# Kernel optimization log

Hardware: AMD Instinct MI355X
Metric: run time of the kernel (lower is better)

The kernel has to match this reference:

```python
import jax, jax.numpy as jnp
import numpy as np

B, A, G = 8, 200000, 64
K = 4                       # max_k: top-k anchors per GT
T_LOW, T_HIGH = 0.3, 0.7    # matcher thresholds
NUM_SAMPLES, POS_FRAC = 256, 0.5  # batch_size_per_image, positive_fraction
MAX_POS = int(NUM_SAMPLES * POS_FRAC)  # 128


def cxcywh_to_xyxy(b):
    cx, cy, w, h = b[..., 0], b[..., 1], b[..., 2], b[..., 3]
    return jnp.stack([cx - 0.5 * w, cy - 0.5 * h, cx + 0.5 * w, cy + 0.5 * h], axis=-1)


def box_iou(b1, b2):
    # b1: [G,4], b2: [A,4] in xyxy -> iou [G,A]
    area1 = (b1[:, 2] - b1[:, 0]) * (b1[:, 3] - b1[:, 1])
    area2 = (b2[:, 2] - b2[:, 0]) * (b2[:, 3] - b2[:, 1])
    lt = jnp.maximum(b1[:, None, :2], b2[None, :, :2])
    rb = jnp.minimum(b1[:, None, 2:], b2[None, :, 2:])
    wh = jnp.clip(rb - lt, 0.0)
    inter = wh[..., 0] * wh[..., 1]
    union = area1[:, None] + area2[None, :] - inter
    return inter / union


def _per_image(anchors, gt, key):
    iou = box_iou(cxcywh_to_xyxy(gt), cxcywh_to_xyxy(anchors))  # [G, A]
    # --- Matcher(thresholds=[t_low, t_high], labels=[0,-1,1], allow_low_quality_matches=True)
    matched_vals = iou.max(axis=0)        # best IoU per anchor
    matches = jnp.argmax(iou, axis=0)     # matched GT per anchor
    labels = jnp.where(matched_vals >= T_HIGH, 1,
             jnp.where(matched_vals >= T_LOW, -1, 0))
    hq = iou.max(axis=1)                  # highest quality per GT
    labels = jnp.where((iou == hq[:, None]).any(axis=0), 1, labels)  # low-quality matches -> positive
    # --- subsample_labels: randomly keep at most 128 positives (negatives don't affect outputs)
    is_pos = labels == 1
    r = jax.random.uniform(key, (anchors.shape[0],))
    rank = jnp.argsort(jnp.argsort(jnp.where(is_pos, r, 2.0)))  # random rank among positives
    num_pos = jnp.minimum(MAX_POS, is_pos.sum())
    sel_pos = is_pos & (rank < num_pos)
    # --- sample_topk_per_gt: per GT keep min(count, K) top-IoU anchors (fixed-shape, padded with -1)
    counts = jax.ops.segment_sum(sel_pos.astype(jnp.int32), matches, num_segments=G)
    top_vals, top_idx = jax.lax.top_k(iou, K)  # [G, K]
    valid = jnp.arange(K)[None, :] < jnp.minimum(counts, K)[:, None]
    pr = jnp.where(valid, top_idx, -1).reshape(-1)
    gt_i = jnp.where(valid, jnp.arange(G)[:, None], -1).reshape(-1)
    scores = jnp.where(valid, top_vals, 0.0).reshape(-1)
    return pr, gt_i, valid.reshape(-1), scores


def setup_inputs() -> dict:
    key = jax.random.key(0)
    k1, k2 = jax.random.split(key)
    anchors = jax.random.uniform(k1, (B, A, 4), dtype=jnp.float32)   # cxcywh
    gt_boxes = jax.random.uniform(k2, (B, G, 4), dtype=jnp.float32)  # cxcywh
    return {"anchors": anchors, "gt_boxes": gt_boxes}


def reference(anchors, gt_boxes):
    # Returns padded (pr_inds, gt_inds, valid_mask, topk_ious), each [B, G*K];
    # invalid slots hold -1 indices (padding for the variable-length torch output).
    keys = jax.random.split(jax.random.key(42), anchors.shape[0])
    return jax.vmap(_per_image)(anchors, gt_boxes, keys)
```

## Files before the change

### kernel.cpp

```cpp
#include <hip/hip_runtime.h>
#include <stdint.h>


#pragma clang fp contract(off)

#define B_IMG 8
#define A_N 200000
#define G_N 64
#define K_TOP 4
#define MAX_POS 128
#define FINE_CAP 4096
#define AS 2048
#define NS 98
#define SUB_SL 16
#define SUB_AS 1024
#define WPS 32
#define NWORD 3136

typedef unsigned long long u64;
typedef unsigned int u32;

__device__ __forceinline__ u32 rotl32(u32 v, int n) { return (v << n) | (v >> (32 - n)); }

__device__ __forceinline__ void tf_round(u32& x0, u32& x1, int r) {
  x0 += x1; x1 = rotl32(x1, r); x1 ^= x0;
}

__device__ __forceinline__ void threefry2x32(u32 k0, u32 k1, u32& x0, u32& x1) {
  u32 ks2 = 0x1BD11BDAu ^ k0 ^ k1;
  x0 += k0; x1 += k1;
  tf_round(x0,x1,13); tf_round(x0,x1,15); tf_round(x0,x1,26); tf_round(x0,x1,6);
  x0 += k1; x1 += ks2 + 1u;
  tf_round(x0,x1,17); tf_round(x0,x1,29); tf_round(x0,x1,16); tf_round(x0,x1,24);
  x0 += ks2; x1 += k0 + 2u;
  tf_round(x0,x1,13); tf_round(x0,x1,15); tf_round(x0,x1,26); tf_round(x0,x1,6);
  x0 += k0; x1 += k1 + 3u;
  tf_round(x0,x1,17); tf_round(x0,x1,29); tf_round(x0,x1,16); tf_round(x0,x1,24);
  x0 += k1; x1 += ks2 + 4u;
  tf_round(x0,x1,13); tf_round(x0,x1,15); tf_round(x0,x1,26); tf_round(x0,x1,6);
  x0 += ks2; x1 += k0 + 5u;
}

__device__ __forceinline__ void image_key(int b, u32& kb0, u32& kb1) {
  u32 x0 = 0u, x1 = (u32)b;
  threefry2x32(0u, 42u, x0, x1);
  kb0 = x0; kb1 = x1;
}

__device__ __forceinline__ u32 rbits_for(u32 k0, u32 k1, u32 a) {
  u32 x0 = 0u, x1 = a;
  threefry2x32(k0, k1, x0, x1);
  return x0 ^ x1;
}

__device__ __forceinline__ void conv_box(float4 bx, float& x0, float& y0,
                                         float& x1, float& y1, float& area) {
  #pragma clang fp contract(off)
  x0 = bx.x - 0.5f * bx.z;
  y0 = bx.y - 0.5f * bx.w;
  x1 = bx.x + 0.5f * bx.z;
  y1 = bx.y + 0.5f * bx.w;
  area = (x1 - x0) * (y1 - y0);
}

__device__ __forceinline__ float iou_pair(float ax0, float ay0, float ax1, float ay1, float aarea,
                                          float gx0, float gy0, float gx1, float gy1, float garea) {
  #pragma clang fp contract(off)
  float ltx = fmaxf(gx0, ax0), lty = fmaxf(gy0, ay0);
  float rbx = fminf(gx1, ax1), rby = fminf(gy1, ay1);
  float w = fmaxf(rbx - ltx, 0.0f), h = fmaxf(rby - lty, 0.0f);
  float inter = w * h;
  float uni = (garea + aarea) - inter;
  return inter / uni;
}

__device__ __forceinline__ void iou_parts(float ax0, float ay0, float ax1, float ay1, float aarea,
                                          float gx0, float gy0, float gx1, float gy1, float garea,
                                          float& inter, float& uni) {
  #pragma clang fp contract(off)
  float ltx = fmaxf(gx0, ax0), lty = fmaxf(gy0, ay0);
  float rbx = fminf(gx1, ax1), rby = fminf(gy1, ay1);
  float w = fmaxf(rbx - ltx, 0.0f), h = fmaxf(rby - lty, 0.0f);
  inter = w * h;
  uni = (garea + aarea) - inter;
}

__device__ __forceinline__ void top4_insert(u64 (&top)[4], u64 key) {
  if (key > top[3]) {
    if (key > top[0])      { top[3]=top[2]; top[2]=top[1]; top[1]=top[0]; top[0]=key; }
    else if (key > top[1]) { top[3]=top[2]; top[2]=top[1]; top[1]=key; }
    else if (key > top[2]) { top[3]=top[2]; top[2]=key; }
    else                   { top[3]=key; }
  }
}

__device__ __forceinline__ void wave_merge_top4(u64 (&top)[4]) {
  for (int off = 32; off >= 1; off >>= 1) {
    u64 o[4];
    #pragma unroll
    for (int k = 0; k < 4; k++) o[k] = __shfl_down(top[k], (unsigned)off);
    u64 m[4]; int i = 0, j = 0;
    #pragma unroll
    for (int k = 0; k < 4; k++) m[k] = (top[i] >= o[j]) ? top[i++] : o[j++];
    #pragma unroll
    for (int k = 0; k < 4; k++) top[k] = m[k];
  }
}

__device__ __forceinline__ void wave_merge_top4_u32(u32 (&top)[4]) {
  for (int off = 32; off >= 1; off >>= 1) {
    u32 o[4];
    #pragma unroll
    for (int k = 0; k < 4; k++) o[k] = __shfl_down(top[k], (unsigned)off);
    u32 m[4]; int i = 0, j = 0;
    #pragma unroll
    for (int k = 0; k < 4; k++) m[k] = (top[i] >= o[j]) ? top[i++] : o[j++];
    #pragma unroll
    for (int k = 0; k < 4; k++) top[k] = m[k];
  }
}

__device__ __forceinline__ float screen_thresh(u32 tau) {
  u32 tb = (tau > 8u) ? (tau - 8u) : 0u;
  return __uint_as_float(tb);
}

__launch_bounds__(512, 4)
__global__ void k_thresh(const float4* __restrict__ anchors, const float4* __restrict__ gt,
                         u32* __restrict__ thr_part, u32* __restrict__ hist,
                         u32* __restrict__ npos, u32* __restrict__ fcnt,
                         u32* __restrict__ cnt,
                         float* __restrict__ out, int sec) {
  const int s = blockIdx.x;
  const int b = blockIdx.y;
  const int half = blockIdx.z;
  const int t = threadIdx.x;
  const int wave = t >> 6, lane = t & 63;

  __shared__ float4 sxy[SUB_AS];
  __shared__ float  sg[5][32];

  {
    int lid = ((half * B_IMG + b) * SUB_SL + s) * 512 + t;
    if (lid < B_IMG * 4096) hist[lid] = 0;
    if (lid < B_IMG * G_N * K_TOP) {
      out[0 * sec + lid] = -1.0f;
      out[1 * sec + lid] = -1.0f;
      out[2 * sec + lid] = 0.0f;
      out[3 * sec + lid] = 0.0f;
    }
  }
  if (s == 0 && half == 0) {
    if (t < 64) cnt[b * G_N + t] = 0;
    if (t == 0) { fcnt[b] = 0; npos[b] = 0; }
  }

  const int base = s * SUB_AS;
  const float4* ab = anchors + (size_t)b * A_N + base;

  for (int j = t; j < SUB_AS; j += 512) {
    float x0, y0, x1, y1, ar;
    conv_box(ab[j], x0, y0, x1, y1, ar);
    sxy[j] = make_float4(x0, y0, x1, y1);
  }
  if (t < 32) {
    float x0, y0, x1, y1, ar;
    conv_box(gt[(size_t)b * G_N + half * 32 + t], x0, y0, x1, y1, ar);
    sg[0][t] = x0; sg[1][t] = y0; sg[2][t] = x1; sg[3][t] = y1; sg[4][t] = ar;
  }
  __syncthreads();

  {
    const int gi = wave * 4;
    const float g0x0 = sg[0][gi],   g0y0 = sg[1][gi],   g0x1 = sg[2][gi],   g0y1 = sg[3][gi],   g0a = sg[4][gi];
    const float g1x0 = sg[0][gi+1], g1y0 = sg[1][gi+1], g1x1 = sg[2][gi+1], g1y1 = sg[3][gi+1], g1a = sg[4][gi+1];
    const float g2x0 = sg[0][gi+2], g2y0 = sg[1][gi+2], g2x1 = sg[2][gi+2], g2y1 = sg[3][gi+2], g2a = sg[4][gi+2];
    const float g3x0 = sg[0][gi+3], g3y0 = sg[1][gi+3], g3x1 = sg[2][gi+3], g3y1 = sg[3][gi+3], g3a = sg[4][gi+3];

    u32 q0 = 0, q1 = 0, q2 = 0, q3 = 0;
    for (int j = lane; j < SUB_AS; j += 64) {
      float4 x = sxy[j];
      float aarea = (x.z - x.x) * (x.w - x.y);
      float i0, u0, i1, u1, i2, u2, i3, u3;
      iou_parts(x.x, x.y, x.z, x.w, aarea, g0x0, g0y0, g0x1, g0y1, g0a, i0, u0);
      iou_parts(x.x, x.y, x.z, x.w, aarea, g1x0, g1y0, g1x1, g1y1, g1a, i1, u1);
      iou_parts(x.x, x.y, x.z, x.w, aarea, g2x0, g2y0, g2x1, g2y1, g2a, i2, u2);
      iou_parts(x.x, x.y, x.z, x.w, aarea, g3x0, g3y0, g3x1, g3y1, g3a, i3, u3);
      q0 = max(q0, __float_as_uint(i0 * __builtin_amdgcn_rcpf(u0)));
      q1 = max(q1, __float_as_uint(i1 * __builtin_amdgcn_rcpf(u1)));
      q2 = max(q2, __float_as_uint(i2 * __builtin_amdgcn_rcpf(u2)));
      q3 = max(q3, __float_as_uint(i3 * __builtin_amdgcn_rcpf(u3)));
    }
    u32 Q0[4] = {q0,0,0,0}, Q1[4] = {q1,0,0,0}, Q2[4] = {q2,0,0,0}, Q3[4] = {q3,0,0,0};
    wave_merge_top4_u32(Q0);
    wave_merge_top4_u32(Q1);
    wave_merge_top4_u32(Q2);
    wave_merge_top4_u32(Q3);
    if (lane == 0) {
      u32* dst = thr_part + ((size_t)b * SUB_SL + s) * G_N + half * 32 + gi;
      dst[0] = Q0[3]; dst[1] = Q1[3]; dst[2] = Q2[3]; dst[3] = Q3[3];
    }
  }
}

__launch_bounds__(512, 4)
__global__ void k_main(const float4* __restrict__ anchors, const float4* __restrict__ gt,
                       const u32* __restrict__ thr_part,
                       u64* __restrict__ partial, u64* __restrict__ posA,
                       u32* __restrict__ hist, u32* __restrict__ npos) {
  const int s = blockIdx.x;
  const int b = blockIdx.y;
  const int t = threadIdx.x;
  const int wave = t >> 6, lane = t & 63;

  __shared__ float4 sxy[AS];
  __shared__ float  sg[5][64];
  __shared__ float  sthr[64];
  u32* wm = (u32*)sxy;

  const int base = s * AS;
  const int acnt = min(AS, A_N - base);
  const float4* ab = anchors + (size_t)b * A_N + base;

  for (int j = t; j < acnt; j += 512) {
    float x0, y0, x1, y1, ar;
    conv_box(ab[j], x0, y0, x1, y1, ar);
    sxy[j] = make_float4(x0, y0, x1, y1);
  }
  if (t < 64) {
    float x0, y0, x1, y1, ar;
    conv_box(gt[(size_t)b * G_N + t], x0, y0, x1, y1, ar);
    sg[0][t] = x0; sg[1][t] = y0; sg[2][t] = x1; sg[3][t] = y1; sg[4][t] = ar;
    u32 mx = 0;
    for (int ss = 0; ss < SUB_SL; ss++)
      mx = max(mx, thr_part[((size_t)b * SUB_SL + ss) * G_N + t]);
    const u32 L7 = 0x3F333333u - 8u;
    sthr[t] = screen_thresh(min(mx > 16u ? mx - 16u : 0u, L7));
  }
  __syncthreads();

  u32 m = 0;
  for (int gg = 0; gg < 2; gg++) {
    const int gp = wave * 2 + gg;
    const int gi = gp * 4;
    const float g0x0 = sg[0][gi],   g0y0 = sg[1][gi],   g0x1 = sg[2][gi],   g0y1 = sg[3][gi],   g0a = sg[4][gi];
    const float g1x0 = sg[0][gi+1], g1y0 = sg[1][gi+1], g1x1 = sg[2][gi+1], g1y1 = sg[3][gi+1], g1a = sg[4][gi+1];
    const float g2x0 = sg[0][gi+2], g2y0 = sg[1][gi+2], g2x1 = sg[2][gi+2], g2y1 = sg[3][gi+2], g2a = sg[4][gi+2];
    const float g3x0 = sg[0][gi+3], g3y0 = sg[1][gi+3], g3x1 = sg[2][gi+3], g3y1 = sg[3][gi+3], g3a = sg[4][gi+3];
    const float t0 = sthr[gi], t1 = sthr[gi+1], t2 = sthr[gi+2], t3 = sthr[gi+3];

    u64 T0[4] = {0,0,0,0}, T1[4] = {0,0,0,0}, T2[4] = {0,0,0,0}, T3[4] = {0,0,0,0};
    u32 h0 = 0, h1 = 0, h2 = 0, h3 = 0;
    u32 bit = 1u;
    for (int j = lane; j < acnt; j += 64, bit <<= 1) {
      float4 x = sxy[j];
      float aarea = (x.z - x.x) * (x.w - x.y);
      float i0, u0, i1, u1, i2, u2, i3, u3;
      iou_parts(x.x, x.y, x.z, x.w, aarea, g0x0, g0y0, g0x1, g0y1, g0a, i0, u0);
      iou_parts(x.x, x.y, x.z, x.w, aarea, g1x0, g1y0, g1x1, g1y1, g1a, i1, u1);
      iou_parts(x.x, x.y, x.z, x.w, aarea, g2x0, g2y0, g2x1, g2y1, g2a, i2, u2);
      iou_parts(x.x, x.y, x.z, x.w, aarea, g3x0, g3y0, g3x1, g3y1, g3a, i3, u3);
      u32 ni = ~(u32)(base + j);
      bool s0 = (i0 >= t0 * u0), s1 = (i1 >= t1 * u1);
      bool s2 = (i2 >= t2 * u2), s3 = (i3 >= t3 * u3);
      if (__ballot(s0)) {
        float v = 0.0f;
        if (s0) { v = i0 / u0; if (v >= 0.7f) m |= bit; }
        u32 vb = __float_as_uint(v);
        bool ins = s0 && (vb >= h0);
        if (__ballot(ins)) {
          if (ins) top4_insert(T0, ((u64)vb << 32) | (u64)ni);
          h0 = (u32)(T0[3] >> 32);
        }
      }
      if (__ballot(s1)) {
        float v = 0.0f;
        if (s1) { v = i1 / u1; if (v >= 0.7f) m |= bit; }
        u32 vb = __float_as_uint(v);
        bool ins = s1 && (vb >= h1);
        if (__ballot(ins)) {
          if (ins) top4_insert(T1, ((u64)vb << 32) | (u64)ni);
          h1 = (u32)(T1[3] >> 32);
        }
      }
      if (__ballot(s2)) {
        float v = 0.0f;
        if (s2) { v = i2 / u2; if (v >= 0.7f) m |= bit; }
        u32 vb = __float_as_uint(v);
        bool ins = s2 && (vb >= h2);
        if (__ballot(ins)) {
          if (ins) top4_insert(T2, ((u64)vb << 32) | (u64)ni);
          h2 = (u32)(T2[3] >> 32);
        }
      }
      if (__ballot(s3)) {
        float v = 0.0f;
        if (s3) { v = i3 / u3; if (v >= 0.7f) m |= bit; }
        u32 vb = __float_as_uint(v);
        bool ins = s3 && (vb >= h3);
        if (__ballot(ins)) {
          if (ins) top4_insert(T3, ((u64)vb << 32) | (u64)ni);
          h3 = (u32)(T3[3] >> 32);
        }
      }
    }
    wave_merge_top4(T0);
    wave_merge_top4(T1);
    wave_merge_top4(T2);
    wave_merge_top4(T3);
    if (lane == 0) {
      u64* dst = partial + (((size_t)b * NS + s) * G_N + gi) * 4;
      #pragma unroll
      for (int k = 0; k < 4; k++) {
        dst[k] = T0[k]; dst[4 + k] = T1[k]; dst[8 + k] = T2[k]; dst[12 + k] = T3[k];
      }
    }
  }

  __syncthreads();
  wm[t] = m;
  __syncthreads();
  if (wave == 0) {
    u32 mc = 0;
    #pragma unroll
    for (int w = 0; w < 8; w++) mc |= wm[w * 64 + lane];
    u64* posH = posA + (size_t)b * NWORD + s * WPS;
    for (int k = 0; k < WPS; k++) {
      u64 bal = __ballot((mc >> k) & 1u);
      if (lane == 0) posH[k] = bal;
    }
    u32 k0, k1; image_key(b, k0, k1);
    u32 c = (u32)__popc(mc);
    u32 mm = mc;
    while (mm) {
      int k = __ffs((int)mm) - 1; mm &= mm - 1;
      u32 a = (u32)(base + k * 64 + lane);
      atomicAdd(&hist[b * 4096 + (rbits_for(k0, k1, a) >> 20)], 1u);
    }
    #pragma unroll
    for (int off = 32; off >= 1; off >>= 1) c += __shfl_xor(c, off);
    if (lane == 0 && c) atomicAdd(&npos[b], c);
  }
}

__launch_bounds__(64)
__global__ void k_top4_merge(const u64* __restrict__ partial, u64* __restrict__ top4,
                             u64* __restrict__ posA,
                             u32* __restrict__ hist, u32* __restrict__ npos) {
  const int b = blockIdx.y, g = blockIdx.x, lane = threadIdx.x;
  const u64* pb = partial + ((size_t)b * NS * G_N + g) * 4;
  u64 keys[7];
  int nk = 0;
  for (int i = lane; i < NS * 4; i += 64)
    keys[nk++] = pb[(size_t)(i >> 2) * (G_N * 4) + (i & 3)];
  u64 top[4] = {0ull, 0ull, 0ull, 0ull};
  for (int q = 0; q < nk; q++) top4_insert(top, keys[q]);
  wave_merge_top4(top);
  if (lane == 0) {
    u64* dst = top4 + ((size_t)b * G_N + g) * 4;
    #pragma unroll
    for (int k = 0; k < 4; k++) dst[k] = top[k];
  }
  u32 hqb = (u32)(__shfl(top[0], 0) >> 32);
  u32 kk0, kk1; image_key(b, kk0, kk1);
  for (int q = 0; q < nk; q++) {
    u64 key = keys[q];
    u32 aidx = ~(u32)key;
    if ((u32)(key >> 32) == hqb && aidx < A_N) {
      u64 bit = 1ull << (aidx & 63);
      u64 old = atomicOr(&posA[(size_t)b * NWORD + (aidx >> 6)], bit);
      if (!(old & bit)) {
        atomicAdd(&hist[b * 4096 + (rbits_for(kk0, kk1, aidx) >> 20)], 1u);
        atomicAdd(&npos[b], 1u);
      }
    }
  }
}

__launch_bounds__(256)
__global__ void k_collect(const u64* __restrict__ posA,
                          const u32* __restrict__ npos, const u32* __restrict__ hist,
                          int2* __restrict__ binsel,
                          u32* __restrict__ fine, u32* __restrict__ fcnt) {
  const int b = blockIdx.y;
  const int t = threadIdx.x;
  __shared__ u32 red[256];
  __shared__ int sbin;

  const u32* hb = hist + b * 4096;
  u32 local = 0;
  for (int j = 0; j < 16; j++) local += hb[t * 16 + j];
  red[t] = local;
  __syncthreads();
  if (t == 0) {
    if (npos[b] <= MAX_POS) {
      sbin = -1;
      binsel[b] = make_int2(-1, 0);
    } else {
      u32 cum = 0; int chunk = 0;
      for (int i = 0; i < 256; i++) {
        if (cum + red[i] >= MAX_POS) { chunk = i; break; }
        cum += red[i];
      }
      int tb = chunk * 16; u32 before = cum;
      for (int j = 0; j < 16; j++) {
        u32 h = hb[chunk * 16 + j];
        if (before + h >= MAX_POS) { tb = chunk * 16 + j; break; }
        before += h;
      }
      sbin = tb;
      binsel[b] = make_int2(tb, (int)before);
    }
  }
  __syncthreads();
  const int stb = sbin;
  if (stb < 0) return;

  u32 k0, k1; image_key(b, k0, k1);
  const int a0 = blockIdx.x * AS;
  const u64* pa = posA + (size_t)b * NWORD;
  for (int j = t; j < AS; j += 256) {
    int a = a0 + j;
    if (a >= A_N) break;
    if (!((pa[a >> 6] >> (a & 63)) & 1ull)) continue;
    u32 rb = rbits_for(k0, k1, (u32)a);
    if ((int)(rb >> 20) != stb) continue;
    u32 idx = atomicAdd(&fcnt[b], 1u);
    if (idx < FINE_CAP) fine[b * FINE_CAP + idx] = (((rb >> 9) & 0x7FFu) << 18) | (u32)a;
  }
}

__launch_bounds__(256)
__global__ void k_count(const float4* __restrict__ anchors, const float4* __restrict__ gt,
                        const u64* __restrict__ posA,
                        const int2* __restrict__ binsel, const u32* __restrict__ fine,
                        const u32* __restrict__ fcnt, u32* __restrict__ cnt,
                        const u64* __restrict__ top4,
                        float* __restrict__ out, int sec) {
  const int b = blockIdx.y;
  const int t = threadIdx.x;
  __shared__ float sg[5][64];
  __shared__ u64 sT;

  if (t < 64) {
    float x0, y0, x1, y1, ar;
    conv_box(gt[(size_t)b * G_N + t], x0, y0, x1, y1, ar);
    sg[0][t] = x0; sg[1][t] = y0; sg[2][t] = x1; sg[3][t] = y1; sg[4][t] = ar;
    int2 bs = binsel[b];
    u64 T = ~0ull;
    if (bs.x >= 0) {
      const int m = min((int)fcnt[b], FINE_CAP);
      const u32 need = (u32)(MAX_POS - bs.y);
      const u32* fb = fine + b * FINE_CAP;
      u32 lo = 0, hi = (1u << 29) - 1;
      while (lo < hi) {
        u32 mid = lo + ((hi - lo) >> 1);
        u32 c = 0;
        for (int j = t; j < m; j += 64) c += (fb[j] <= mid) ? 1u : 0u;
        #pragma unroll
        for (int off = 32; off >= 1; off >>= 1) c += __shfl_xor(c, off);
        if (c >= need) hi = mid; else lo = mid + 1;
      }
      T = ((u64)(u32)bs.x << 29) | (u64)lo;
    }
    if (t == 0) sT = T;
  }
  __syncthreads();

  u32 k0, k1; image_key(b, k0, k1);
  const u64 T = sT;
  const int a0 = blockIdx.x * AS;
  const u64* pa = posA + (size_t)b * NWORD;
  const float4* ab = anchors + (size_t)b * A_N;
  for (int j = t; j < AS; j += 256) {
    int a = a0 + j;
    if (a >= A_N) break;
    if (!((pa[a >> 6] >> (a & 63)) & 1ull)) continue;
    if (T != ~0ull) {
      u32 rb = rbits_for(k0, k1, (u32)a);
      if (((((u64)(rb >> 9)) << 18) | (u64)(u32)a) > T) continue;
    }
    float ax0, ay0, ax1, ay1, aar;
    conv_box(ab[a], ax0, ay0, ax1, ay1, aar);
    float bv = -1.0f; int g0 = 0;
    for (int g = 0; g < 64; g++) {
      float v = iou_pair(ax0, ay0, ax1, ay1, aar,
                         sg[0][g], sg[1][g], sg[2][g], sg[3][g], sg[4][g]);
      if (v > bv) { bv = v; g0 = g; }
    }
    u32 r = atomicAdd(&cnt[b * G_N + g0], 1u);
    if (r < (u32)K_TOP) {
      u64 key = top4[((size_t)b * G_N + g0) * 4 + r];
      u32 fb4 = (u32)(key >> 32);
      u32 aidx = ~(u32)key;
      int o = b * (G_N * K_TOP) + g0 * K_TOP + (int)r;
      out[0 * sec + o] = (float)aidx;
      out[1 * sec + o] = (float)g0;
      out[2 * sec + o] = 1.0f;
      out[3 * sec + o] = __uint_as_float(fb4);
    }
  }
}

extern "C" void kernel_launch(void* const* d_in, const int* in_sizes, int n_in,
                              void* d_out, int out_size, void* d_ws, size_t ws_size,
                              hipStream_t stream) {
  const float4* anchors = (const float4*)d_in[0];
  const float4* gt      = (const float4*)d_in[1];
  float* out = (float*)d_out;

  char* ws = (char*)d_ws;
  u64*  top4    = (u64*)(ws);
  u64*  partial = (u64*)(ws + 16384);
  u32*  fine    = (u32*)(ws + 16384);
  int2* binsel  = (int2*)(ws + 147456);
  u64*  posA    = (u64*)(ws + 1622016);
  u32*  hist    = (u32*)(ws + 1822720);
  u32*  npos    = (u32*)(ws + 1953792);
  u32*  fcnt    = (u32*)(ws + 1953824);
  u32*  cnt     = (u32*)(ws + 1953856);
  u32*  thr_prt = (u32*)(ws + 1955904);

  int sec = out_size / 4;

  k_thresh    <<<dim3(SUB_SL, B_IMG, 2), 512, 0, stream>>>(anchors, gt, thr_prt, hist, npos, fcnt, cnt, out, sec);
  k_main      <<<dim3(NS, B_IMG), 512, 0, stream>>>(anchors, gt, thr_prt, partial, posA, hist, npos);
  k_top4_merge<<<dim3(G_N, B_IMG), 64, 0, stream>>>(partial, top4, posA, hist, npos);
  k_collect   <<<dim3(NS, B_IMG), 256, 0, stream>>>(posA, npos, hist, binsel, fine, fcnt);
  k_count     <<<dim3(NS, B_IMG), 256, 0, stream>>>(anchors, gt, posA, binsel, fine, fcnt, cnt, top4, out, sec);
}
```

Before: 250.5 us.

## Hoist per-image bin selection and threshold search into tiny dedicated kernels

The histogram bin selection and the binary search for the positive-rank threshold were recomputed redundantly by every block of k_collect and k_count (98 blocks per image). They now run once per image in two small single-wavefront kernels, k_bin and k_tstar, whose results go to workspace for the big kernels to read. This removes the repeated serial prefix scans and the ~29-step binary search from the critical path of each block. The cost is two extra kernel launches and dependencies in the stream.

```diff
diff --git a/kernel.cpp b/kernel.cpp
--- a/kernel.cpp
+++ b/kernel.cpp
@@ -377,24 +377,22 @@
   }
 }
 
-__launch_bounds__(256)
-__global__ void k_collect(const u64* __restrict__ posA,
-                          const u32* __restrict__ npos, const u32* __restrict__ hist,
-                          int2* __restrict__ binsel,
-                          u32* __restrict__ fine, u32* __restrict__ fcnt) {
-  const int b = blockIdx.y;
-  const int t = threadIdx.x;
+__launch_bounds__(64)
+__global__ void k_bin(const u32* __restrict__ npos, const u32* __restrict__ hist,
+                      int2* __restrict__ binsel) {
+  const int b = blockIdx.x;
+  const int lane = threadIdx.x;
   __shared__ u32 red[256];
-  __shared__ int sbin;
 
   const u32* hb = hist + b * 4096;
-  u32 local = 0;
-  for (int j = 0; j < 16; j++) local += hb[t * 16 + j];
-  red[t] = local;
+  for (int c = lane * 4; c < lane * 4 + 4; c++) {
+    u32 s = 0;
+    for (int j = 0; j < 16; j++) s += hb[c * 16 + j];
+    red[c] = s;
+  }
   __syncthreads();
-  if (t == 0) {
+  if (lane == 0) {
     if (npos[b] <= MAX_POS) {
-      sbin = -1;
       binsel[b] = make_int2(-1, 0);
     } else {
       u32 cum = 0; int chunk = 0;
@@ -408,12 +406,18 @@
         if (before + h >= MAX_POS) { tb = chunk * 16 + j; break; }
         before += h;
       }
-      sbin = tb;
       binsel[b] = make_int2(tb, (int)before);
     }
   }
-  __syncthreads();
-  const int stb = sbin;
+}
+
+__launch_bounds__(256)
+__global__ void k_collect(const u64* __restrict__ posA,
+                          const int2* __restrict__ binsel,
+                          u32* __restrict__ fine, u32* __restrict__ fcnt) {
+  const int b = blockIdx.y;
+  const int t = threadIdx.x;
+  const int stb = binsel[b].x;
   if (stb < 0) return;
 
   u32 k0, k1; image_key(b, k0, k1);
@@ -430,45 +434,50 @@
   }
 }
 
+__launch_bounds__(64)
+__global__ void k_tstar(const int2* __restrict__ binsel, const u32* __restrict__ fine,
+                        const u32* __restrict__ fcnt, u64* __restrict__ tstar) {
+  const int b = blockIdx.x;
+  const int lane = threadIdx.x;
+  int2 bs = binsel[b];
+  u64 T = ~0ull;
+  if (bs.x >= 0) {
+    const int m = min((int)fcnt[b], FINE_CAP);
+    const u32 need = (u32)(MAX_POS - bs.y);
+    const u32* fb = fine + b * FINE_CAP;
+    u32 lo = 0, hi = (1u << 29) - 1;
+    while (lo < hi) {
+      u32 mid = lo + ((hi - lo) >> 1);
+      u32 c = 0;
+      for (int j = lane; j < m; j += 64) c += (fb[j] <= mid) ? 1u : 0u;
+      #pragma unroll
+      for (int off = 32; off >= 1; off >>= 1) c += __shfl_xor(c, off);
+      if (c >= need) hi = mid; else lo = mid + 1;
+    }
+    T = ((u64)(u32)bs.x << 29) | (u64)lo;
+  }
+  if (lane == 0) tstar[b] = T;
+}
+
 __launch_bounds__(256)
 __global__ void k_count(const float4* __restrict__ anchors, const float4* __restrict__ gt,
                         const u64* __restrict__ posA,
-                        const int2* __restrict__ binsel, const u32* __restrict__ fine,
-                        const u32* __restrict__ fcnt, u32* __restrict__ cnt,
+                        const u64* __restrict__ tstar, u32* __restrict__ cnt,
                         const u64* __restrict__ top4,
                         float* __restrict__ out, int sec) {
   const int b = blockIdx.y;
   const int t = threadIdx.x;
   __shared__ float sg[5][64];
-  __shared__ u64 sT;
 
   if (t < 64) {
     float x0, y0, x1, y1, ar;
     conv_box(gt[(size_t)b * G_N + t], x0, y0, x1, y1, ar);
     sg[0][t] = x0; sg[1][t] = y0; sg[2][t] = x1; sg[3][t] = y1; sg[4][t] = ar;
-    int2 bs = binsel[b];
-    u64 T = ~0ull;
-    if (bs.x >= 0) {
-      const int m = min((int)fcnt[b], FINE_CAP);
-      const u32 need = (u32)(MAX_POS - bs.y);
-      const u32* fb = fine + b * FINE_CAP;
-      u32 lo = 0, hi = (1u << 29) - 1;
-      while (lo < hi) {
-        u32 mid = lo + ((hi - lo) >> 1);
-        u32 c = 0;
-        for (int j = t; j < m; j += 64) c += (fb[j] <= mid) ? 1u : 0u;
-        #pragma unroll
-        for (int off = 32; off >= 1; off >>= 1) c += __shfl_xor(c, off);
-        if (c >= need) hi = mid; else lo = mid + 1;
-      }
-      T = ((u64)(u32)bs.x << 29) | (u64)lo;
-    }
-    if (t == 0) sT = T;
   }
   __syncthreads();
 
   u32 k0, k1; image_key(b, k0, k1);
-  const u64 T = sT;
+  const u64 T = tstar[b];
   const int a0 = blockIdx.x * AS;
   const u64* pa = posA + (size_t)b * NWORD;
   const float4* ab = anchors + (size_t)b * A_N;
@@ -520,12 +529,15 @@
   u32*  fcnt    = (u32*)(ws + 1953824);
   u32*  cnt     = (u32*)(ws + 1953856);
   u32*  thr_prt = (u32*)(ws + 1955904);
+  u64*  tstar   = (u64*)(ws + 1988672);
 
   int sec = out_size / 4;
 
   k_thresh    <<<dim3(SUB_SL, B_IMG, 2), 512, 0, stream>>>(anchors, gt, thr_prt, hist, npos, fcnt, cnt, out, sec);
   k_main      <<<dim3(NS, B_IMG), 512, 0, stream>>>(anchors, gt, thr_prt, partial, posA, hist, npos);
   k_top4_merge<<<dim3(G_N, B_IMG), 64, 0, stream>>>(partial, top4, posA, hist, npos);
-  k_collect   <<<dim3(NS, B_IMG), 256, 0, stream>>>(posA, npos, hist, binsel, fine, fcnt);
-  k_count     <<<dim3(NS, B_IMG), 256, 0, stream>>>(anchors, gt, posA, binsel, fine, fcnt, cnt, top4, out, sec);
-}
+  k_bin       <<<dim3(B_IMG), 64, 0, stream>>>(npos, hist, binsel);
+  k_collect   <<<dim3(NS, B_IMG), 256, 0, stream>>>(posA, binsel, fine, fcnt);
+  k_tstar     <<<dim3(B_IMG), 64, 0, stream>>>(binsel, fine, fcnt, tstar);
+  k_count     <<<dim3(NS, B_IMG), 256, 0, stream>>>(anchors, gt, posA, tstar, cnt, top4, out, sec);
+}
```

Result: no change. 252.7 us (+0.9%).
